# Kernel optimization log

Measured on AMD Instinct MI355X. Metric: run time of the kernel, lower is better.

The kernel has to match this reference:

```python
import jax, jax.numpy as jnp
import numpy as np

B, S, N, F, H, O = 16, 64, 256, 64, 1, 64
NEG_SLOPE = 0.2  # PyG GATConv default leaky_relu slope


def setup_inputs() -> dict:
    key = jax.random.key(0)
    ks = jax.random.split(key, 6)
    x = jax.random.normal(ks[0], (B, S, N, F), dtype=jnp.float32)
    adj = jax.random.randint(ks[1], (B, S, N, N), 0, 2, dtype=jnp.int32)
    W = jax.random.normal(ks[2], (F, H * O), dtype=jnp.float32) * 0.1
    att_src = jax.random.normal(ks[3], (H, O), dtype=jnp.float32) * 0.1
    att_dst = jax.random.normal(ks[4], (H, O), dtype=jnp.float32) * 0.1
    bias = jnp.zeros((H * O,), dtype=jnp.float32)
    return {"x": x, "adj": adj, "W": W, "att_src": att_src,
            "att_dst": att_dst, "bias": bias}


def reference(x, adj, W, att_src, att_dst, bias):
    b, s, n, f = x.shape
    h_, o_ = att_src.shape
    # linear transform: [B,S,N,H,O]
    h = (x @ W).reshape(b, s, n, h_, o_)
    a_s = jnp.einsum('bsnho,ho->bsnh', h, att_src)  # per-source score
    a_d = jnp.einsum('bsnho,ho->bsnh', h, att_dst)  # per-target score
    # e[b,s,i,j,h]: raw attention for edge source j -> target i
    e = jax.nn.leaky_relu(a_d[:, :, :, None, :] + a_s[:, :, None, :, :],
                          NEG_SLOPE)
    # dense_to_sparse: edge (row=src j, col=tgt i) where adj[j,i] != 0;
    # GATConv removes then re-adds self-loops -> diagonal always present.
    neigh = jnp.swapaxes(adj, -1, -2) != 0          # [B,S,i,j]
    mask = neigh | jnp.eye(n, dtype=bool)
    neg = jnp.finfo(e.dtype).min
    e = jnp.where(mask[..., None], e, neg)
    alpha = jax.nn.softmax(e, axis=3)               # softmax over sources j
    out = jnp.einsum('bsijh,bsjho->bsiho', alpha, h)
    return out.reshape(b, s, n, h_ * o_) + bias
```

## Files before the change

### kernel.cpp

```cpp
#include <hip/hip_runtime.h>
#include <math.h>


constexpr int NN = 256;
constexpr int FF = 64;
constexpr int OO = 64;

constexpr int OFF_HT   = 0;
constexpr int OFF_AL   = 32768;
constexpr int OFF_MASK = 43008;
constexpr int OFF_AS   = 51200;
constexpr int OFF_INVL = 52224;
constexpr int OFF_RED  = 53248;
constexpr int SMEM_TOTAL = 53264;

typedef _Float16 half4 __attribute__((ext_vector_type(4)));
typedef float f32x4 __attribute__((ext_vector_type(4)));

__global__ __launch_bounds__(256, 3) void gat_fused(
    const float* __restrict__ x,
    const int*   __restrict__ adj,
    const float* __restrict__ W,
    const float* __restrict__ att_src,
    const float* __restrict__ att_dst,
    const float* __restrict__ bias,
    float* __restrict__ out)
{
    __shared__ __align__(16) unsigned char smem[SMEM_TOTAL];
    _Float16* hT            = (_Float16*)(smem + OFF_HT);
    _Float16* al            = (_Float16*)(smem + OFF_AL);
    unsigned long long* m64 = (unsigned long long*)(smem + OFF_MASK);
    const unsigned* m32     = (const unsigned*)(smem + OFF_MASK);
    float* as_s             = (float*)(smem + OFF_AS);
    float* invl_s           = (float*)(smem + OFF_INVL);
    float* red_s            = (float*)(smem + OFF_RED);

    const int tid  = threadIdx.x;
    const int bs   = blockIdx.x;
    const int lane = tid & 63;
    const int wv   = tid >> 6;

    const float* xg   = x + (size_t)bs * NN * FF;
    const int4*  adjv = reinterpret_cast<const int4*>(adj + (size_t)bs * NN * NN);
    float*       outg = out + (size_t)bs * NN * OO;

    #pragma unroll
    for (int cc = 0; cc < 8; ++cc) {
        int4 v[8];
        #pragma unroll
        for (int k = 0; k < 8; ++k)
            v[k] = adjv[(wv * 64 + cc * 8 + k) * 64 + lane];
        #pragma unroll
        for (int k = 0; k < 8; ++k) {
            const int j = wv * 64 + cc * 8 + k;
            unsigned long long bb[4];
            bb[0] = __ballot(v[k].x != 0);
            bb[1] = __ballot(v[k].y != 0);
            bb[2] = __ballot(v[k].z != 0);
            bb[3] = __ballot(v[k].w != 0);
            bb[k & 3] |= 1ull << (wv * 16 + cc * 2 + (k >> 2));
            if (lane < 4) {
                unsigned long long bv = (lane == 0) ? bb[0] : (lane == 1) ? bb[1]
                                      : (lane == 2) ? bb[2] : bb[3];
                m64[j * 4 + lane] = bv;
            }
        }
    }

    float acc[OO];
    #pragma unroll
    for (int o = 0; o < OO; ++o) acc[o] = 0.f;

    const float4* xv = reinterpret_cast<const float4*>(xg + tid * FF);
    const float4* Wv = reinterpret_cast<const float4*>(W);
    for (int k4 = 0; k4 < FF / 4; ++k4) {
        float4 xq = xv[k4];
        float xs[4] = {xq.x, xq.y, xq.z, xq.w};
        #pragma unroll
        for (int kk = 0; kk < 4; ++kk) {
            float xk = xs[kk];
            const float4* wrow = Wv + (k4 * 4 + kk) * (OO / 4);
            #pragma unroll
            for (int o4 = 0; o4 < OO / 4; ++o4) {
                float4 w = wrow[o4];
                acc[o4 * 4 + 0] = fmaf(xk, w.x, acc[o4 * 4 + 0]);
                acc[o4 * 4 + 1] = fmaf(xk, w.y, acc[o4 * 4 + 1]);
                acc[o4 * 4 + 2] = fmaf(xk, w.z, acc[o4 * 4 + 2]);
                acc[o4 * 4 + 3] = fmaf(xk, w.w, acc[o4 * 4 + 3]);
            }
        }
    }

    float as_i = 0.f, ad_i = 0.f;
    {
        const float4* sv = reinterpret_cast<const float4*>(att_src);
        const float4* dv = reinterpret_cast<const float4*>(att_dst);
        #pragma unroll
        for (int o4 = 0; o4 < OO / 4; ++o4) {
            float4 a = sv[o4], d = dv[o4];
            as_i += acc[o4*4+0]*a.x + acc[o4*4+1]*a.y + acc[o4*4+2]*a.z + acc[o4*4+3]*a.w;
            ad_i += acc[o4*4+0]*d.x + acc[o4*4+1]*d.y + acc[o4*4+2]*d.z + acc[o4*4+3]*d.w;
        }
    }
    as_s[tid] = as_i;
    #pragma unroll
    for (int o = 0; o < OO; ++o) {
        int boff = o * 512 + ((2 * tid) ^ ((o & 7) << 4));
        *(_Float16*)(smem + OFF_HT + boff) = (_Float16)acc[o];
    }

    float vmax = as_i;
    #pragma unroll
    for (int off = 32; off > 0; off >>= 1)
        vmax = fmaxf(vmax, __shfl_xor(vmax, off));
    if (lane == 0) red_s[wv] = vmax;

    __syncthreads();

    const float smax = fmaxf(fmaxf(red_s[0], red_s[1]), fmaxf(red_s[2], red_s[3]));
    float mm = ad_i + smax;
    mm = fmaxf(mm, 0.2f * mm);
    const float adm = ad_i - mm;
    const float c2  = fmaf(0.2f, ad_i, -mm);

    const int woff = ((tid & 3) << 1) + (tid >> 7);
    const int bitp = (tid >> 2) & 31;
    const int r = lane & 15;
    const int g = lane >> 4;

    const int albase = tid * 40;
    int afbase[4];
    #pragma unroll
    for (int c = 0; c < 4; ++c)
        afbase[c] = (wv * 64 + c * 16 + r) * 40 + g * 8;
    int bfbase[4];
    const int lo = (g * 8) ^ ((r & 1) << 4);
    const int xh = ((r >> 1) & 3) * 32;
    #pragma unroll
    for (int nc = 0; nc < 4; ++nc)
        bfbase[nc] = (nc * 16 + r) * 512 + lo;

    f32x4 dacc[4][4];
    #pragma unroll
    for (int c = 0; c < 4; ++c)
        #pragma unroll
        for (int nc = 0; nc < 4; ++nc)
            dacc[c][nc] = (f32x4){0.f, 0.f, 0.f, 0.f};

    float lacc[4] = {0.f, 0.f, 0.f, 0.f};

    #pragma unroll
    for (int t = 0; t < 16; ++t) {
        #pragma unroll
        for (int q = 0; q < 4; ++q) {
            half4 hq;
            #pragma unroll
            for (int e = 0; e < 4; ++e) {
                const int j = t * 16 + q * 4 + e;
                unsigned w = m32[j * 8 + woff];
                float aj = as_s[j];
                float u  = adm + aj;
                float vv = fmaf(0.2f, aj, c2);
                float ev = fmaxf(u, vv);
                float pf = __expf(ev);
                bool valid = (w >> bitp) & 1u;
                pf = valid ? pf : 0.f;
                lacc[e] += pf;
                hq[e] = (_Float16)pf;
            }
            *(half4*)(smem + OFF_AL + albase + q * 8) = hq;
        }
        asm volatile("" ::: "memory");

        half4 bf[4];
        const int kx = (t * 32) ^ xh;
        #pragma unroll
        for (int nc = 0; nc < 4; ++nc)
            bf[nc] = *(const half4*)(smem + OFF_HT + bfbase[nc] + kx);
        #pragma unroll
        for (int c = 0; c < 4; ++c) {
            half4 af = *(const half4*)(smem + OFF_AL + afbase[c]);
            #pragma unroll
            for (int nc = 0; nc < 4; ++nc)
                dacc[c][nc] = __builtin_amdgcn_mfma_f32_16x16x16f16(
                    af, bf[nc], dacc[c][nc], 0, 0, 0);
        }
    }

    const float l = (lacc[0] + lacc[1]) + (lacc[2] + lacc[3]);
    invl_s[tid] = 1.0f / l;
    asm volatile("" ::: "memory");

    float bl[4];
    #pragma unroll
    for (int nc = 0; nc < 4; ++nc) bl[nc] = bias[nc * 16 + r];

    #pragma unroll
    for (int c = 0; c < 4; ++c) {
        #pragma unroll
        for (int q = 0; q < 4; ++q) {
            const int i_row = wv * 64 + c * 16 + g * 4 + q;
            float ir = invl_s[i_row];
            float* orow = outg + (size_t)i_row * OO;
            #pragma unroll
            for (int nc = 0; nc < 4; ++nc)
                orow[nc * 16 + r] = fmaf(dacc[c][nc][q], ir, bl[nc]);
        }
    }
}

extern "C" void kernel_launch(void* const* d_in, const int* in_sizes, int n_in,
                              void* d_out, int out_size, void* d_ws, size_t ws_size,
                              hipStream_t stream) {
    const float* x        = (const float*)d_in[0];
    const int*   adj      = (const int*)  d_in[1];
    const float* W        = (const float*)d_in[2];
    const float* att_src  = (const float*)d_in[3];
    const float* att_dst  = (const float*)d_in[4];
    const float* bias     = (const float*)d_in[5];
    float*       out      = (float*)d_out;

    dim3 grid(1024);
    dim3 block(256);
    hipLaunchKernelGGL(gat_fused, grid, block, 0, stream,
                       x, adj, W, att_src, att_dst, bias, out);
}
```

Measured before the change: 130.9 us.

## Stream adjacency per column into registers and shrink LDS staging

Drops the up-front ballot pass that packed the whole adjacency into an LDS bitmask. Each thread now loads its own adjacency column directly, 16 rows per tile, prefetching the next tile into registers. The alpha staging buffer becomes per-wave and is written in two half-wave phases interleaved with the MFMAs, and 1/l moves through shuffles instead of LDS. Less LDS allows 4 blocks per CU, but the column loads are strided int reads (lanes coalesce across j but each load is only 4 bytes) and register pressure rises.

```diff
diff --git a/kernel.cpp b/kernel.cpp
--- a/kernel.cpp
+++ b/kernel.cpp
@@ -6,18 +6,16 @@
 constexpr int FF = 64;
 constexpr int OO = 64;
 
-constexpr int OFF_HT   = 0;
-constexpr int OFF_AL   = 32768;
-constexpr int OFF_MASK = 43008;
-constexpr int OFF_AS   = 51200;
-constexpr int OFF_INVL = 52224;
-constexpr int OFF_RED  = 53248;
-constexpr int SMEM_TOTAL = 53264;
+constexpr int OFF_HT  = 0;
+constexpr int OFF_AL  = 32768;
+constexpr int OFF_AS  = 37888;
+constexpr int OFF_RED = 38912;
+constexpr int SMEM_TOTAL = 38928;
 
 typedef _Float16 half4 __attribute__((ext_vector_type(4)));
 typedef float f32x4 __attribute__((ext_vector_type(4)));
 
-__global__ __launch_bounds__(256, 3) void gat_fused(
+__global__ __launch_bounds__(256, 4) void gat_fused(
     const float* __restrict__ x,
     const int*   __restrict__ adj,
     const float* __restrict__ W,
@@ -27,13 +25,8 @@
     float* __restrict__ out)
 {
     __shared__ __align__(16) unsigned char smem[SMEM_TOTAL];
-    _Float16* hT            = (_Float16*)(smem + OFF_HT);
-    _Float16* al            = (_Float16*)(smem + OFF_AL);
-    unsigned long long* m64 = (unsigned long long*)(smem + OFF_MASK);
-    const unsigned* m32     = (const unsigned*)(smem + OFF_MASK);
-    float* as_s             = (float*)(smem + OFF_AS);
-    float* invl_s           = (float*)(smem + OFF_INVL);
-    float* red_s            = (float*)(smem + OFF_RED);
+    float* as_s  = (float*)(smem + OFF_AS);
+    float* red_s = (float*)(smem + OFF_RED);
 
     const int tid  = threadIdx.x;
     const int bs   = blockIdx.x;
@@ -41,31 +34,8 @@
     const int wv   = tid >> 6;
 
     const float* xg   = x + (size_t)bs * NN * FF;
-    const int4*  adjv = reinterpret_cast<const int4*>(adj + (size_t)bs * NN * NN);
+    const int*   adjg = adj + (size_t)bs * NN * NN;
     float*       outg = out + (size_t)bs * NN * OO;
-
-    #pragma unroll
-    for (int cc = 0; cc < 8; ++cc) {
-        int4 v[8];
-        #pragma unroll
-        for (int k = 0; k < 8; ++k)
-            v[k] = adjv[(wv * 64 + cc * 8 + k) * 64 + lane];
-        #pragma unroll
-        for (int k = 0; k < 8; ++k) {
-            const int j = wv * 64 + cc * 8 + k;
-            unsigned long long bb[4];
-            bb[0] = __ballot(v[k].x != 0);
-            bb[1] = __ballot(v[k].y != 0);
-            bb[2] = __ballot(v[k].z != 0);
-            bb[3] = __ballot(v[k].w != 0);
-            bb[k & 3] |= 1ull << (wv * 16 + cc * 2 + (k >> 2));
-            if (lane < 4) {
-                unsigned long long bv = (lane == 0) ? bb[0] : (lane == 1) ? bb[1]
-                                      : (lane == 2) ? bb[2] : bb[3];
-                m64[j * 4 + lane] = bv;
-            }
-        }
-    }
 
     float acc[OO];
     #pragma unroll
@@ -123,22 +93,20 @@
     const float adm = ad_i - mm;
     const float c2  = fmaf(0.2f, ad_i, -mm);
 
-    const int woff = ((tid & 3) << 1) + (tid >> 7);
-    const int bitp = (tid >> 2) & 31;
     const int r = lane & 15;
     const int g = lane >> 4;
 
-    const int albase = tid * 40;
-    int afbase[4];
-    #pragma unroll
-    for (int c = 0; c < 4; ++c)
-        afbase[c] = (wv * 64 + c * 16 + r) * 40 + g * 8;
-    int bfbase[4];
+    const int alw   = OFF_AL + wv * 1280;
+    const int wbase = alw + (tid & 31) * 40;
+    const bool hi   = (tid & 32) != 0;
+    const int afb0  = alw + r * 40 + g * 8;
+    const int afb1  = alw + (16 + r) * 40 + g * 8;
+
     const int lo = (g * 8) ^ ((r & 1) << 4);
     const int xh = ((r >> 1) & 3) * 32;
-    #pragma unroll
-    for (int nc = 0; nc < 4; ++nc)
-        bfbase[nc] = (nc * 16 + r) * 512 + lo;
+    int bfb[4];
+    #pragma unroll
+    for (int nc = 0; nc < 4; ++nc) bfb[nc] = OFF_HT + (nc * 16 + r) * 512 + lo;
 
     f32x4 dacc[4][4];
     #pragma unroll
@@ -149,47 +117,87 @@
 
     float lacc[4] = {0.f, 0.f, 0.f, 0.f};
 
+    const int* adjcol = adjg + tid;
+    int av[16];
+    #pragma unroll
+    for (int e = 0; e < 16; ++e) av[e] = adjcol[e * NN];
+
     #pragma unroll
     for (int t = 0; t < 16; ++t) {
+        int avn[16];
+        if (t < 15) {
+            #pragma unroll
+            for (int e = 0; e < 16; ++e)
+                avn[e] = adjcol[(t + 1) * 16 * NN + e * NN];
+        }
+
+        half4 pq[4];
         #pragma unroll
         for (int q = 0; q < 4; ++q) {
-            half4 hq;
+            float4 a4 = *(const float4*)&as_s[t * 16 + q * 4];
+            float as4[4] = {a4.x, a4.y, a4.z, a4.w};
+            half4 hv;
             #pragma unroll
             for (int e = 0; e < 4; ++e) {
                 const int j = t * 16 + q * 4 + e;
-                unsigned w = m32[j * 8 + woff];
-                float aj = as_s[j];
+                float aj = as4[e];
                 float u  = adm + aj;
                 float vv = fmaf(0.2f, aj, c2);
                 float ev = fmaxf(u, vv);
                 float pf = __expf(ev);
-                bool valid = (w >> bitp) & 1u;
+                bool valid = (av[q * 4 + e] != 0) || (j == tid);
                 pf = valid ? pf : 0.f;
                 lacc[e] += pf;
-                hq[e] = (_Float16)pf;
+                hv[e] = (_Float16)pf;
             }
-            *(half4*)(smem + OFF_AL + albase + q * 8) = hq;
-        }
-        asm volatile("" ::: "memory");
+            pq[q] = hv;
+        }
 
         half4 bf[4];
         const int kx = (t * 32) ^ xh;
         #pragma unroll
         for (int nc = 0; nc < 4; ++nc)
-            bf[nc] = *(const half4*)(smem + OFF_HT + bfbase[nc] + kx);
-        #pragma unroll
-        for (int c = 0; c < 4; ++c) {
-            half4 af = *(const half4*)(smem + OFF_AL + afbase[c]);
+            bf[nc] = *(const half4*)(smem + bfb[nc] + kx);
+
+        if (!hi) {
+            #pragma unroll
+            for (int q = 0; q < 4; ++q)
+                *(half4*)(smem + wbase + q * 8) = pq[q];
+        }
+        asm volatile("" ::: "memory");
+        #pragma unroll
+        for (int c = 0; c < 2; ++c) {
+            half4 af = *(const half4*)(smem + (c ? afb1 : afb0));
             #pragma unroll
             for (int nc = 0; nc < 4; ++nc)
                 dacc[c][nc] = __builtin_amdgcn_mfma_f32_16x16x16f16(
                     af, bf[nc], dacc[c][nc], 0, 0, 0);
         }
+        asm volatile("" ::: "memory");
+        if (hi) {
+            #pragma unroll
+            for (int q = 0; q < 4; ++q)
+                *(half4*)(smem + wbase + q * 8) = pq[q];
+        }
+        asm volatile("" ::: "memory");
+        #pragma unroll
+        for (int c = 2; c < 4; ++c) {
+            half4 af = *(const half4*)(smem + ((c & 1) ? afb1 : afb0));
+            #pragma unroll
+            for (int nc = 0; nc < 4; ++nc)
+                dacc[c][nc] = __builtin_amdgcn_mfma_f32_16x16x16f16(
+                    af, bf[nc], dacc[c][nc], 0, 0, 0);
+        }
+        asm volatile("" ::: "memory");
+
+        if (t < 15) {
+            #pragma unroll
+            for (int e = 0; e < 16; ++e) av[e] = avn[e];
+        }
     }
 
     const float l = (lacc[0] + lacc[1]) + (lacc[2] + lacc[3]);
-    invl_s[tid] = 1.0f / l;
-    asm volatile("" ::: "memory");
+    const float invl = 1.0f / l;
 
     float bl[4];
     #pragma unroll
@@ -199,8 +207,9 @@
     for (int c = 0; c < 4; ++c) {
         #pragma unroll
         for (int q = 0; q < 4; ++q) {
-            const int i_row = wv * 64 + c * 16 + g * 4 + q;
-            float ir = invl_s[i_row];
+            const int rsel = c * 16 + g * 4 + q;
+            float ir = __shfl(invl, rsel, 64);
+            const int i_row = wv * 64 + rsel;
             float* orow = outg + (size_t)i_row * OO;
             #pragma unroll
             for (int nc = 0; nc < 4; ++nc)
```

New measurement: 277.5 us. +112.1%, slower.
